# Kernel optimization log

Measured on AMD Instinct MI355X. Metric: run time of the kernel, lower is better.

## Reference

```python
import jax, jax.numpy as jnp
import numpy as np
from math import pi

N = 262144
OUT_RES = 512
OUT_CHANNELS = 64
EPS = 3.33  # out_res in [177, 890)
SQ2PI = 2.50662827463


def make_sphere_pos(out_res, eps):
    # Fibonacci sphere lattice, matches the torch buffer construction.
    indices = jnp.arange(out_res, dtype=jnp.float32)
    golden_ratio = (1 + 5 ** 0.5) / 2
    phi = jnp.arccos(1 - 2 * (indices + eps) / (out_res - 1 + 2 * eps))
    theta = 2 * pi * indices / golden_ratio
    x = jnp.cos(theta) * jnp.sin(phi)
    y = jnp.sin(theta) * jnp.sin(phi)
    z = jnp.cos(phi)
    return jnp.stack([x, y, z], axis=0).astype(jnp.float32)  # [3, out_res]


def setup_inputs() -> dict:
    key = jax.random.key(0)
    k1, k2 = jax.random.split(key)
    vec = jax.random.normal(k1, (N, 3), dtype=jnp.float32)
    vec = vec / (jnp.linalg.norm(vec, axis=-1, keepdims=True) + 1e-8)  # unit directions
    weights = jax.random.uniform(k2, (1, OUT_RES, OUT_CHANNELS), dtype=jnp.float32)
    sphere_pos = make_sphere_pos(OUT_RES, EPS)
    sigma = jnp.full((1,), 0.1, dtype=jnp.float32)
    return {"vec": vec, "sphere_pos": sphere_pos, "weights": weights, "sigma": sigma}


def reference(vec, sphere_pos, weights, sigma):
    # cos_dist: [N, out_res]
    cos_dist = jnp.clip(vec @ sphere_pos, -1 + 1e-5, 1 - 1e-5)
    ang = jnp.arccos(cos_dist)
    prob = jnp.exp(-(ang / sigma) ** 2 / 2) / SQ2PI / sigma  # gaussian of geodesic dist
    prob = prob / (prob.sum(axis=1, keepdims=True) + 1e-8)
    # [N, out_res] @ [out_res, out_channels] -> [N, out_channels]
    return prob @ weights[0]
```

## Files before the change

kernel.cpp:

```cpp
#include <hip/hip_runtime.h>

typedef short bf16x8 __attribute__((ext_vector_type(8)));
typedef float f32x4  __attribute__((ext_vector_type(4)));

__device__ __forceinline__ unsigned short f2bf_rne(float x) {
  union { float f; unsigned u; } a; a.f = x;
  unsigned r = a.u + 0x7fffu + ((a.u >> 16) & 1u);
  return (unsigned short)(r >> 16);
}

__device__ __forceinline__ float fast_exp2(float x) {
#if __has_builtin(__builtin_amdgcn_exp2f)
  return __builtin_amdgcn_exp2f(x);
#else
  float r; asm("v_exp_f32 %0, %1" : "=v"(r) : "v"(x)); return r;
#endif
}

__device__ __forceinline__ unsigned cvt_pk_bf16(float a, float b) {
  unsigned r; asm("v_cvt_pk_bf16_f32 %0, %1, %2" : "=v"(r) : "v"(a), "v"(b)); return r;
}

__global__ __launch_bounds__(1024, 4) void sph_enc_kernel(
    const float* __restrict__ vec,
    const float* __restrict__ sph,
    const float* __restrict__ wts,
    const float* __restrict__ sigp,
    float* __restrict__ out)
{
  __shared__ __align__(16) unsigned char wlds[64 * 512 * 2];
  __shared__ __align__(16) float slds[3 * 512];

  const int tid  = threadIdx.x;
  const int lane = tid & 63;
  const int wave = tid >> 6;

  for (int i = tid; i < 1536; i += 1024) slds[i] = sph[i];

  {
    const int c    = tid & 63;
    const int kgrp = tid >> 6;
    const int swz  = (c & 7) << 4;
    #pragma unroll
    for (int pass = 0; pass < 4; ++pass) {
      const int k0 = pass * 128 + (kgrp << 3);
      unsigned pk[4];
      #pragma unroll
      for (int i = 0; i < 4; ++i) {
        const unsigned lo = f2bf_rne(wts[(k0 + 2 * i)     * 64 + c]);
        const unsigned hi = f2bf_rne(wts[(k0 + 2 * i + 1) * 64 + c]);
        pk[i] = lo | (hi << 16);
      }
      *reinterpret_cast<uint4*>(wlds + (((c << 10) + (k0 << 1)) ^ swz)) =
          make_uint4(pk[0], pk[1], pk[2], pk[3]);
    }
  }
  __syncthreads();

  const float sigma = sigp[0];
  const float C1 = -1.44269504f / (sigma * sigma);
  const float C2 = C1 * 0.16666667f;
  const float K2 = -__log2f(2.50662827463f * sigma);

  const int r16  = lane & 15;
  const int q    = lane >> 4;
  const int row0 = (blockIdx.x << 9) + (wave << 4) + r16;
  const int row1 = row0 + 256;

  const float nvx0 = -vec[row0 * 3 + 0];
  const float nvy0 = -vec[row0 * 3 + 1];
  const float nvz0 = -vec[row0 * 3 + 2];
  const float nvx1 = -vec[row1 * 3 + 0];
  const float nvy1 = -vec[row1 * 3 + 1];
  const float nvz1 = -vec[row1 * 3 + 2];

  f32x4 acc0[4], acc1[4];
  #pragma unroll
  for (int nb = 0; nb < 4; ++nb) {
    acc0[nb] = (f32x4){0.f, 0.f, 0.f, 0.f};
    acc1[nb] = (f32x4){0.f, 0.f, 0.f, 0.f};
  }
  float rsa0 = 0.f, rsb0 = 0.f, rsa1 = 0.f, rsb1 = 0.f;

  const int swz_r = (lane & 7) << 4;

  #pragma unroll
  for (int kt = 0; kt < 16; ++kt) {
    const int j0 = kt * 32 + q * 8;
    union { bf16x8 v; unsigned u32[4]; } af0, af1;

    #pragma unroll
    for (int h = 0; h < 2; ++h) {
      const int jh = j0 + 4 * h;
      const f32x4 X = *reinterpret_cast<const f32x4*>(&slds[jh]);
      const f32x4 Y = *reinterpret_cast<const f32x4*>(&slds[512 + jh]);
      const f32x4 Z = *reinterpret_cast<const f32x4*>(&slds[1024 + jh]);
      float p[4];
      #pragma unroll
      for (int e = 0; e < 4; ++e) {
        const float u = fmaf(nvx0, X[e], fmaf(nvy0, Y[e], fmaf(nvz0, Z[e], 1.0f)));
        p[e] = fast_exp2(fmaf(u, fmaf(u, C2, C1), K2));
      }
      rsa0 += p[0] + p[2];
      rsb0 += p[1] + p[3];
      af0.u32[2 * h]     = cvt_pk_bf16(p[0], p[1]);
      af0.u32[2 * h + 1] = cvt_pk_bf16(p[2], p[3]);
      #pragma unroll
      for (int e = 0; e < 4; ++e) {
        const float u = fmaf(nvx1, X[e], fmaf(nvy1, Y[e], fmaf(nvz1, Z[e], 1.0f)));
        p[e] = fast_exp2(fmaf(u, fmaf(u, C2, C1), K2));
      }
      rsa1 += p[0] + p[2];
      rsb1 += p[1] + p[3];
      af1.u32[2 * h]     = cvt_pk_bf16(p[0], p[1]);
      af1.u32[2 * h + 1] = cvt_pk_bf16(p[2], p[3]);
    }

    const int kbyte = j0 << 1;
    #pragma unroll
    for (int nb = 0; nb < 4; ++nb) {
      const bf16x8 bf = *reinterpret_cast<const bf16x8*>(
          wlds + (((((nb << 4) + r16) << 10) + kbyte) ^ swz_r));
      acc0[nb] = __builtin_amdgcn_mfma_f32_16x16x32_bf16(af0.v, bf, acc0[nb], 0, 0, 0);
      acc1[nb] = __builtin_amdgcn_mfma_f32_16x16x32_bf16(af1.v, bf, acc1[nb], 0, 0, 0);
    }
  }

  float rsum0 = rsa0 + rsb0;
  float rsum1 = rsa1 + rsb1;
  rsum0 += __shfl_xor(rsum0, 16);
  rsum0 += __shfl_xor(rsum0, 32);
  rsum1 += __shfl_xor(rsum1, 16);
  rsum1 += __shfl_xor(rsum1, 32);

  const int obase = (blockIdx.x << 9) + (wave << 4);
  #pragma unroll
  for (int reg = 0; reg < 4; ++reg) {
    const int orow = (q << 2) + reg;
    const float rinv0 = 1.0f / (__shfl(rsum0, orow) + 1e-8f);
    const float rinv1 = 1.0f / (__shfl(rsum1, orow) + 1e-8f);
    const int b0 = ((obase + orow) << 6) + r16;
    const int b1 = ((obase + 256 + orow) << 6) + r16;
    out[b0 +  0] = acc0[0][reg] * rinv0;
    out[b0 + 16] = acc0[1][reg] * rinv0;
    out[b0 + 32] = acc0[2][reg] * rinv0;
    out[b0 + 48] = acc0[3][reg] * rinv0;
    out[b1 +  0] = acc1[0][reg] * rinv1;
    out[b1 + 16] = acc1[1][reg] * rinv1;
    out[b1 + 32] = acc1[2][reg] * rinv1;
    out[b1 + 48] = acc1[3][reg] * rinv1;
  }
}

extern "C" void kernel_launch(void* const* d_in, const int* in_sizes, int n_in,
                              void* d_out, int out_size, void* d_ws, size_t ws_size,
                              hipStream_t stream) {
  const float* vec = (const float*)d_in[0];
  const float* sph = (const float*)d_in[1];
  const float* wts = (const float*)d_in[2];
  const float* sig = (const float*)d_in[3];
  float* out = (float*)d_out;
  const int n      = in_sizes[0] / 3;
  const int blocks = n >> 9;
  hipLaunchKernelGGL(sph_enc_kernel, dim3(blocks), dim3(1024), 0, stream,
                     vec, sph, wts, sig, out);
}
```

Measured before the change: 48.96 us.

## Sort rows by z and skip sphere-point tiles outside the Gaussian window

Result: slower. 84.79 us (+73.2%).

```diff
diff --git a/kernel.cpp b/kernel.cpp
--- a/kernel.cpp
+++ b/kernel.cpp
@@ -1,4 +1,5 @@
 #include <hip/hip_runtime.h>
+#include <math.h>
 
 typedef short bf16x8 __attribute__((ext_vector_type(8)));
 typedef float f32x4  __attribute__((ext_vector_type(4)));
@@ -19,6 +20,206 @@
 
 __device__ __forceinline__ unsigned cvt_pk_bf16(float a, float b) {
   unsigned r; asm("v_cvt_pk_bf16_f32 %0, %1, %2" : "=v"(r) : "v"(a), "v"(b)); return r;
+}
+
+__device__ __forceinline__ int zkey(float vz) {
+  int k = (int)((1.0f - vz) * 128.0f);
+  return min(max(k, 0), 255);
+}
+
+__global__ void hist_k(const float* __restrict__ vec, int* __restrict__ cnt, int rpb) {
+  __shared__ int h[256];
+  h[threadIdx.x] = 0;
+  __syncthreads();
+  const int base = blockIdx.x * rpb;
+  for (int t = threadIdx.x; t < rpb; t += 256)
+    atomicAdd(&h[zkey(vec[(base + t) * 3 + 2])], 1);
+  __syncthreads();
+  cnt[blockIdx.x * 256 + threadIdx.x] = h[threadIdx.x];
+}
+
+__global__ void scan_k(const int* __restrict__ cnt, int* __restrict__ basem) {
+  __shared__ int binbase[257];
+  const int b = threadIdx.x;
+  int run = 0;
+  for (int blk = 0; blk < 256; ++blk) {
+    basem[blk * 256 + b] = run;
+    run += cnt[blk * 256 + b];
+  }
+  __shared__ int tot[256];
+  tot[b] = run;
+  __syncthreads();
+  if (b == 0) {
+    int s = 0;
+    for (int i = 0; i < 256; ++i) { binbase[i] = s; s += tot[i]; }
+  }
+  __syncthreads();
+  const int bb = binbase[b];
+  for (int blk = 0; blk < 256; ++blk) basem[blk * 256 + b] += bb;
+}
+
+__global__ void scatter_k(const float* __restrict__ vec, const int* __restrict__ basem,
+                          int* __restrict__ perm, int rpb) {
+  __shared__ int l[256];
+  l[threadIdx.x] = 0;
+  __syncthreads();
+  const int base = blockIdx.x * rpb;
+  for (int t = threadIdx.x; t < rpb; t += 256) {
+    const int i = base + t;
+    const int k = zkey(vec[i * 3 + 2]);
+    const int r = atomicAdd(&l[k], 1);
+    perm[basem[blockIdx.x * 256 + k] + r] = i;
+  }
+}
+
+__global__ __launch_bounds__(1024, 4) void sph_enc_sorted(
+    const float* __restrict__ vec,
+    const float* __restrict__ sph,
+    const float* __restrict__ wts,
+    const float* __restrict__ sigp,
+    const int*   __restrict__ perm,
+    float* __restrict__ out)
+{
+  __shared__ __align__(16) unsigned char wlds[64 * 512 * 2];
+  __shared__ __align__(16) float slds[3 * 512];
+
+  const int tid  = threadIdx.x;
+  const int lane = tid & 63;
+  const int wave = tid >> 6;
+
+  for (int i = tid; i < 1536; i += 1024) slds[i] = sph[i];
+
+  {
+    const int c    = tid & 63;
+    const int kgrp = tid >> 6;
+    const int swz  = (c & 7) << 4;
+    #pragma unroll
+    for (int pass = 0; pass < 4; ++pass) {
+      const int k0 = pass * 128 + (kgrp << 3);
+      unsigned pk[4];
+      #pragma unroll
+      for (int i = 0; i < 4; ++i) {
+        const unsigned lo = f2bf_rne(wts[(k0 + 2 * i)     * 64 + c]);
+        const unsigned hi = f2bf_rne(wts[(k0 + 2 * i + 1) * 64 + c]);
+        pk[i] = lo | (hi << 16);
+      }
+      *reinterpret_cast<uint4*>(wlds + (((c << 10) + (k0 << 1)) ^ swz)) =
+          make_uint4(pk[0], pk[1], pk[2], pk[3]);
+    }
+  }
+  __syncthreads();
+
+  const float sigma = sigp[0];
+  const float C1 = -1.44269504f / (sigma * sigma);
+  const float C2 = C1 * 0.16666667f;
+  const float K2 = -__log2f(2.50662827463f * sigma);
+
+  const int r16  = lane & 15;
+  const int q    = lane >> 4;
+  const int obase = (blockIdx.x << 9) + (wave << 4);
+  const int p0 = perm[obase + r16];
+  const int p1 = perm[obase + 256 + r16];
+
+  const float vx0 = vec[p0 * 3 + 0], vy0 = vec[p0 * 3 + 1], vz0 = vec[p0 * 3 + 2];
+  const float vx1 = vec[p1 * 3 + 0], vy1 = vec[p1 * 3 + 1], vz1 = vec[p1 * 3 + 2];
+  const float nvx0 = -vx0, nvy0 = -vy0, nvz0 = -vz0;
+  const float nvx1 = -vx1, nvy1 = -vy1, nvz1 = -vz1;
+
+  const float thm = fminf(4.0f * sigma, 3.14159f);
+  const float ct = __cosf(thm), st = __sinf(thm);
+  const float s0 = sqrtf(fmaxf(0.0f, 1.0f - vz0 * vz0));
+  const float s1 = sqrtf(fmaxf(0.0f, 1.0f - vz1 * vz1));
+  float zh = fmaxf(fmaf(vz0, ct, s0 * st), fmaf(vz1, ct, s1 * st));
+  float zl = fminf(fmaf(vz0, ct, -s0 * st), fmaf(vz1, ct, -s1 * st));
+  #pragma unroll
+  for (int m = 1; m < 64; m <<= 1) {
+    zh = fmaxf(zh, __shfl_xor(zh, m));
+    zl = fminf(zl, __shfl_xor(zl, m));
+  }
+  const float Dl = 511.0f + 2.0f * 3.33f;
+  const float fi_lo = (1.0f - zh) * (0.5f * Dl) - 3.33f - 1.5f;
+  const float fi_hi = (1.0f - zl) * (0.5f * Dl) - 3.33f + 1.5f;
+  const int ilo = (int)fmaxf(fi_lo, 0.0f);
+  const int ihi = (int)fminf(fi_hi, 511.0f);
+  const int kt_lo = ilo >> 5;
+  const int kt_hi = (ihi >> 5) + 1;
+
+  f32x4 acc0[4], acc1[4];
+  #pragma unroll
+  for (int nb = 0; nb < 4; ++nb) {
+    acc0[nb] = (f32x4){0.f, 0.f, 0.f, 0.f};
+    acc1[nb] = (f32x4){0.f, 0.f, 0.f, 0.f};
+  }
+  float rsa0 = 0.f, rsb0 = 0.f, rsa1 = 0.f, rsb1 = 0.f;
+
+  const int swz_r = (lane & 7) << 4;
+
+  for (int kt = kt_lo; kt < kt_hi; ++kt) {
+    const int j0 = kt * 32 + q * 8;
+    union { bf16x8 v; unsigned u32[4]; } af0, af1;
+
+    #pragma unroll
+    for (int h = 0; h < 2; ++h) {
+      const int jh = j0 + 4 * h;
+      const f32x4 X = *reinterpret_cast<const f32x4*>(&slds[jh]);
+      const f32x4 Y = *reinterpret_cast<const f32x4*>(&slds[512 + jh]);
+      const f32x4 Z = *reinterpret_cast<const f32x4*>(&slds[1024 + jh]);
+      float p[4];
+      #pragma unroll
+      for (int e = 0; e < 4; ++e) {
+        const float u = fmaf(nvx0, X[e], fmaf(nvy0, Y[e], fmaf(nvz0, Z[e], 1.0f)));
+        p[e] = fast_exp2(fmaf(u, fmaf(u, C2, C1), K2));
+      }
+      rsa0 += p[0] + p[2];
+      rsb0 += p[1] + p[3];
+      af0.u32[2 * h]     = cvt_pk_bf16(p[0], p[1]);
+      af0.u32[2 * h + 1] = cvt_pk_bf16(p[2], p[3]);
+      #pragma unroll
+      for (int e = 0; e < 4; ++e) {
+        const float u = fmaf(nvx1, X[e], fmaf(nvy1, Y[e], fmaf(nvz1, Z[e], 1.0f)));
+        p[e] = fast_exp2(fmaf(u, fmaf(u, C2, C1), K2));
+      }
+      rsa1 += p[0] + p[2];
+      rsb1 += p[1] + p[3];
+      af1.u32[2 * h]     = cvt_pk_bf16(p[0], p[1]);
+      af1.u32[2 * h + 1] = cvt_pk_bf16(p[2], p[3]);
+    }
+
+    const int kbyte = j0 << 1;
+    #pragma unroll
+    for (int nb = 0; nb < 4; ++nb) {
+      const bf16x8 bf = *reinterpret_cast<const bf16x8*>(
+          wlds + (((((nb << 4) + r16) << 10) + kbyte) ^ swz_r));
+      acc0[nb] = __builtin_amdgcn_mfma_f32_16x16x32_bf16(af0.v, bf, acc0[nb], 0, 0, 0);
+      acc1[nb] = __builtin_amdgcn_mfma_f32_16x16x32_bf16(af1.v, bf, acc1[nb], 0, 0, 0);
+    }
+  }
+
+  float rsum0 = rsa0 + rsb0;
+  float rsum1 = rsa1 + rsb1;
+  rsum0 += __shfl_xor(rsum0, 16);
+  rsum0 += __shfl_xor(rsum0, 32);
+  rsum1 += __shfl_xor(rsum1, 16);
+  rsum1 += __shfl_xor(rsum1, 32);
+
+  #pragma unroll
+  for (int reg = 0; reg < 4; ++reg) {
+    const int orow = (q << 2) + reg;
+    const float rinv0 = 1.0f / (__shfl(rsum0, orow) + 1e-8f);
+    const float rinv1 = 1.0f / (__shfl(rsum1, orow) + 1e-8f);
+    const int r0 = perm[obase + orow];
+    const int r1 = perm[obase + 256 + orow];
+    const int b0 = (r0 << 6) + r16;
+    const int b1 = (r1 << 6) + r16;
+    out[b0 +  0] = acc0[0][reg] * rinv0;
+    out[b0 + 16] = acc0[1][reg] * rinv0;
+    out[b0 + 32] = acc0[2][reg] * rinv0;
+    out[b0 + 48] = acc0[3][reg] * rinv0;
+    out[b1 +  0] = acc1[0][reg] * rinv1;
+    out[b1 + 16] = acc1[1][reg] * rinv1;
+    out[b1 + 32] = acc1[2][reg] * rinv1;
+    out[b1 + 48] = acc1[3][reg] * rinv1;
+  }
 }
 
 __global__ __launch_bounds__(1024, 4) void sph_enc_kernel(
@@ -36,7 +237,6 @@
   const int wave = tid >> 6;
 
   for (int i = tid; i < 1536; i += 1024) slds[i] = sph[i];
-
   {
     const int c    = tid & 63;
     const int kgrp = tid >> 6;
@@ -81,14 +281,12 @@
     acc1[nb] = (f32x4){0.f, 0.f, 0.f, 0.f};
   }
   float rsa0 = 0.f, rsb0 = 0.f, rsa1 = 0.f, rsb1 = 0.f;
-
   const int swz_r = (lane & 7) << 4;
 
   #pragma unroll
   for (int kt = 0; kt < 16; ++kt) {
     const int j0 = kt * 32 + q * 8;
     union { bf16x8 v; unsigned u32[4]; } af0, af1;
-
     #pragma unroll
     for (int h = 0; h < 2; ++h) {
       const int jh = j0 + 4 * h;
@@ -115,7 +313,6 @@
       af1.u32[2 * h]     = cvt_pk_bf16(p[0], p[1]);
       af1.u32[2 * h + 1] = cvt_pk_bf16(p[2], p[3]);
     }
-
     const int kbyte = j0 << 1;
     #pragma unroll
     for (int nb = 0; nb < 4; ++nb) {
@@ -160,8 +357,21 @@
   const float* wts = (const float*)d_in[2];
   const float* sig = (const float*)d_in[3];
   float* out = (float*)d_out;
-  const int n      = in_sizes[0] / 3;
-  const int blocks = n >> 9;
-  hipLaunchKernelGGL(sph_enc_kernel, dim3(blocks), dim3(1024), 0, stream,
-                     vec, sph, wts, sig, out);
-}
+  const int n = in_sizes[0] / 3;
+
+  const size_t need = ((size_t)n + 65536 + 65536) * sizeof(int);
+  if (n == 262144 && ws_size >= need) {
+    int* perm  = (int*)d_ws;
+    int* cnt   = perm + n;
+    int* basem = cnt + 65536;
+    const int rpb = n / 256;
+    hipLaunchKernelGGL(hist_k,    dim3(256), dim3(256), 0, stream, vec, cnt, rpb);
+    hipLaunchKernelGGL(scan_k,    dim3(1),   dim3(256), 0, stream, cnt, basem);
+    hipLaunchKernelGGL(scatter_k, dim3(256), dim3(256), 0, stream, vec, basem, perm, rpb);
+    hipLaunchKernelGGL(sph_enc_sorted, dim3(n >> 9), dim3(1024), 0, stream,
+                       vec, sph, wts, sig, perm, out);
+  } else {
+    hipLaunchKernelGGL(sph_enc_kernel, dim3(n >> 9), dim3(1024), 0, stream,
+                       vec, sph, wts, sig, out);
+  }
+}
```
